# Optimization experiments

Hardware: AMD Instinct MI355X
Metric: run time of the kernel (lower is better)

The kernel has to match this reference:

```python
import jax, jax.numpy as jnp
import numpy as np


def setup_inputs() -> dict:
    key = jax.random.key(0)
    k1, k2, k3 = jax.random.split(key, 3)
    N1, N2, D = 2048, 32768, 1024
    return {
        "query_seq": jax.random.normal(k1, (N1, D), dtype=jnp.float32),
        "matching_set": jax.random.normal(k2, (N2, D), dtype=jnp.float32),
        "synth_set": jax.random.normal(k3, (N2, D), dtype=jnp.float32),
        "topk": 4,
    }


def reference(query_seq, matching_set, synth_set, topk):
    # fast_cosine_dist: the torch code computes dot products via the
    # -cdist^2 + ||a||^2 + ||b||^2 identity; mathematically this is q @ m^T.
    q_norm = jnp.linalg.norm(query_seq, axis=-1)        # [N1]
    m_norm = jnp.linalg.norm(matching_set, axis=-1)     # [N2]
    dotprod = jnp.einsum('nd,md->nm', query_seq, matching_set)  # [N1, N2]
    dists = 1.0 - dotprod / (q_norm[:, None] * m_norm[None, :])
    # topk smallest distances -> top_k of negated dists
    _, idx = jax.lax.top_k(-dists, topk)                # [N1, topk]
    out_feats = synth_set[idx].mean(axis=1)             # [N1, D]
    return out_feats
```

## Files before the change

### kernel.cpp

```cpp
#include <hip/hip_runtime.h>

#define N1 2048
#define N2 32768
#define DD 1024
#define BM 128
#define BN 128
#define BK 128
#define NBN (N2 / BN)
#define NBM (N1 / BM)
#define KT  (DD / BK)

typedef __attribute__((ext_vector_type(8))) int   i32x8;
typedef __attribute__((ext_vector_type(4))) int   i32x4;
typedef __attribute__((ext_vector_type(4))) float f32x4;

typedef const __attribute__((address_space(1))) void gv_t;
typedef __attribute__((address_space(3))) void       lv_t;

__device__ __forceinline__ void gload16(const void* g, void* l) {
  __builtin_amdgcn_global_load_lds((gv_t*)g, (lv_t*)l, 16, 0, 0);
}

__device__ __forceinline__ unsigned ordf(float x) {
  union { float f; unsigned u; } a; a.f = x;
  return a.u ^ ((unsigned)((int)a.u >> 31) | 0x80000000u);
}

__global__ __launch_bounds__(256) void nrmcvt8(const float* __restrict__ src,
                                               unsigned char* __restrict__ dst,
                                               float* __restrict__ invn) {
  const int row = blockIdx.x, t = threadIdx.x;
  const float4* s4 = (const float4*)(src + (size_t)row * DD);
  float4 v = s4[t];
  float ss = v.x * v.x + v.y * v.y + v.z * v.z + v.w * v.w;
  #pragma unroll
  for (int o = 32; o > 0; o >>= 1) ss += __shfl_down(ss, o, 64);
  __shared__ float red[4];
  if ((t & 63) == 0) red[t >> 6] = ss;
  __syncthreads();
  float inv = 1.0f / sqrtf(red[0] + red[1] + red[2] + red[3]);
  float sc = inv * 16.0f;
  int p = 0;
  p = __builtin_amdgcn_cvt_pk_fp8_f32(v.x * sc, v.y * sc, p, false);
  p = __builtin_amdgcn_cvt_pk_fp8_f32(v.z * sc, v.w * sc, p, true);
  ((unsigned*)(dst + (size_t)row * DD))[t] = (unsigned)p;
  if (invn != nullptr && t == 0) invn[row] = inv;
}

__global__ __launch_bounds__(256, 2) void gemm_topk(
    const unsigned char* __restrict__ qb,
    const unsigned char* __restrict__ mbn,
    unsigned* __restrict__ cand_k) {
  __shared__ char lds[65536];
  const int tid  = threadIdx.x;
  const int lane = tid & 63;
  const int w = tid >> 6, wr = w >> 1, wc = w & 1;

  int bid = blockIdx.x;
  int swz = (bid & 7) * (NBM * NBN / 8) + (bid >> 3);
  const int bm = swz >> 8;
  const int bn = swz & (NBN - 1);

  {
    int amt = (bid * 37) & 15;
    for (int k = 0; k < amt; ++k) __builtin_amdgcn_s_sleep(1);
  }

  const char* aG = (const char*)(qb  + (size_t)bm * BM * DD);
  const char* bG = (const char*)(mbn + (size_t)bn * BN * DD);

  f32x4 acc[4][4] = {};

  auto stage = [&](int d, int kt) {
    #pragma unroll
    for (int it = 0; it < 4; ++it) {
      int p = it * 256 + tid;
      int r = p >> 3, c = p & 7, cs = c ^ (r & 7);
      gload16(aG + (size_t)r * DD + kt * BK + cs * 16,
              lds + d * 32768 + p * 16);
    }
    #pragma unroll
    for (int it = 0; it < 4; ++it) {
      int p = it * 256 + tid;
      int r = p >> 3, c = p & 7, cs = c ^ (r & 7);
      gload16(bG + (size_t)r * DD + kt * BK + cs * 16,
              lds + d * 32768 + 16384 + p * 16);
    }
  };

  auto compute = [&](int d) {
    const char* Abuf = lds + d * 32768;
    const char* Bbuf = Abuf + 16384;
    const int g2 = 2 * (lane >> 4);
    i32x8 af[4], bb[4];
    #pragma unroll
    for (int i = 0; i < 4; ++i) {
      int ra = wr * 64 + i * 16 + (lane & 15);
      i32x4 lo = *(const i32x4*)(Abuf + ra * 128 + ((g2 ^ (ra & 7)) * 16));
      i32x4 hi = *(const i32x4*)(Abuf + ra * 128 + (((g2 + 1) ^ (ra & 7)) * 16));
      af[i] = __builtin_shufflevector(lo, hi, 0, 1, 2, 3, 4, 5, 6, 7);
      int rb = wc * 64 + i * 16 + (lane & 15);
      i32x4 blo = *(const i32x4*)(Bbuf + rb * 128 + ((g2 ^ (rb & 7)) * 16));
      i32x4 bhi = *(const i32x4*)(Bbuf + rb * 128 + (((g2 + 1) ^ (rb & 7)) * 16));
      bb[i] = __builtin_shufflevector(blo, bhi, 0, 1, 2, 3, 4, 5, 6, 7);
    }
    #pragma unroll
    for (int i = 0; i < 4; ++i)
      #pragma unroll
      for (int j = 0; j < 4; ++j)
        acc[i][j] = __builtin_amdgcn_mfma_scale_f32_16x16x128_f8f6f4(
            af[i], bb[j], acc[i][j], 0 , 0 ,
            0, 0x7F7F7F7F, 0, 0x7F7F7F7F );
  };

  stage(0, 0);
  __syncthreads();
  #pragma unroll 1
  for (int t = 0; t < KT; ++t) {
    if (t + 1 < KT) stage((t + 1) & 1, t + 1);
    compute(t & 1);
    __syncthreads();
  }

  float* sc = (float*)lds;
  #pragma unroll
  for (int i = 0; i < 4; ++i)
    #pragma unroll
    for (int j = 0; j < 4; ++j)
      #pragma unroll
      for (int q = 0; q < 4; ++q) {
        int r = wr * 64 + i * 16 + (lane >> 4) * 4 + q;
        int c = wc * 64 + j * 16 + (lane & 15);
        sc[r * 128 + ((c + r) & 127)] = acc[i][j][q];
      }
  __syncthreads();

  const int srow = tid >> 1, strip = tid & 1;
  unsigned k0 = 0, k1 = 0, k2 = 0, k3 = 0;
  for (int i = 0; i < 64; ++i) {
    int c = strip * 64 + i;
    float s = sc[srow * 128 + ((c + srow) & 127)];
    unsigned key = (ordf(s) & 0xFFFF8000u) | (unsigned)(bn * BN + c);
    unsigned b = key, t2;
    t2 = k0 < b ? k0 : b; k0 = k0 < b ? b : k0; b = t2;
    t2 = k1 < b ? k1 : b; k1 = k1 < b ? b : k1; b = t2;
    t2 = k2 < b ? k2 : b; k2 = k2 < b ? b : k2; b = t2;
    k3 = k3 < b ? b : k3;
  }
  unsigned* dst = cand_k + (size_t)(bm * BM + srow) * (NBN * 8) + bn * 8 + strip * 4;
  *(uint4*)dst = make_uint4(k0, k1, k2, k3);
}

__global__ __launch_bounds__(256) void finalize(
    const float* __restrict__ q, const float* __restrict__ m,
    const float* __restrict__ synth, const unsigned* __restrict__ cand_k,
    const float* __restrict__ inv_mn, float* __restrict__ out) {
  const int lane = threadIdx.x & 63;
  const int row  = blockIdx.x * 4 + (threadIdx.x >> 6);

  uint4 kk[8];
  const uint4* kp = (const uint4*)(cand_k + (size_t)row * (NBN * 8));
  #pragma unroll
  for (int ii = 0; ii < 8; ++ii) kk[ii] = kp[ii * 64 + lane];

  const float4* qp = (const float4*)(q + (size_t)row * DD);
  float4 qv[4];
  #pragma unroll
  for (int ph = 0; ph < 4; ++ph) qv[ph] = qp[ph * 64 + lane];

  unsigned wk[16];
  #pragma unroll
  for (int it = 0; it < 16; ++it) {
    unsigned lm = 0;
    #pragma unroll
    for (int ii = 0; ii < 8; ++ii) {
      unsigned a = kk[ii].x > kk[ii].y ? kk[ii].x : kk[ii].y;
      unsigned b = kk[ii].z > kk[ii].w ? kk[ii].z : kk[ii].w;
      a = a > b ? a : b;
      lm = lm > a ? lm : a;
    }
    #pragma unroll
    for (int o = 1; o < 64; o <<= 1) {
      unsigned other = (unsigned)__shfl_xor((int)lm, o, 64);
      lm = lm > other ? lm : other;
    }
    wk[it] = lm;
    #pragma unroll
    for (int ii = 0; ii < 8; ++ii) {
      kk[ii].x = kk[ii].x == lm ? 0u : kk[ii].x;
      kk[ii].y = kk[ii].y == lm ? 0u : kk[ii].y;
      kk[ii].z = kk[ii].z == lm ? 0u : kk[ii].z;
      kk[ii].w = kk[ii].w == lm ? 0u : kk[ii].w;
    }
  }

  float cosv[16]; int gidx[16];
  #pragma unroll
  for (int it = 0; it < 16; ++it) {
    int g = (int)(wk[it] & 0x7FFFu);
    gidx[it] = g;
    const float4* mp = (const float4*)(m + (size_t)g * DD);
    float d = 0.f;
    #pragma unroll
    for (int ph = 0; ph < 4; ++ph) {
      float4 mv = mp[ph * 64 + lane];
      d += mv.x * qv[ph].x + mv.y * qv[ph].y + mv.z * qv[ph].z + mv.w * qv[ph].w;
    }
    #pragma unroll
    for (int o = 1; o < 64; o <<= 1) d += __shfl_xor(d, o, 64);
    cosv[it] = d * inv_mn[g];
  }

  int sel[4]; bool used[16] = {};
  #pragma unroll
  for (int s = 0; s < 4; ++s) {
    float bv = -1e30f; int bg = 0x7FFFFFFF; int bj = -1;
    #pragma unroll
    for (int j = 0; j < 16; ++j) {
      bool better = !used[j] && (cosv[j] > bv || (cosv[j] == bv && gidx[j] < bg));
      bv = better ? cosv[j] : bv;
      bg = better ? gidx[j] : bg;
      bj = better ? j : bj;
    }
    sel[s] = bg;
    #pragma unroll
    for (int j = 0; j < 16; ++j) used[j] = used[j] || (j == bj);
  }

  const float4* s0 = (const float4*)(synth + (size_t)sel[0] * DD);
  const float4* s1 = (const float4*)(synth + (size_t)sel[1] * DD);
  const float4* s2 = (const float4*)(synth + (size_t)sel[2] * DD);
  const float4* s3 = (const float4*)(synth + (size_t)sel[3] * DD);
  float4* op = (float4*)(out + (size_t)row * DD);
  #pragma unroll
  for (int ph = 0; ph < 4; ++ph) {
    int ix = ph * 64 + lane;
    float4 a = s0[ix], b = s1[ix], c = s2[ix], d = s3[ix];
    float4 r;
    r.x = (a.x + b.x + c.x + d.x) * 0.25f;
    r.y = (a.y + b.y + c.y + d.y) * 0.25f;
    r.z = (a.z + b.z + c.z + d.z) * 0.25f;
    r.w = (a.w + b.w + c.w + d.w) * 0.25f;
    op[ix] = r;
  }
}

extern "C" void kernel_launch(void* const* d_in, const int* in_sizes, int n_in,
                              void* d_out, int out_size, void* d_ws, size_t ws_size,
                              hipStream_t stream) {
  (void)in_sizes; (void)n_in; (void)out_size; (void)ws_size;
  const float* q = (const float*)d_in[0];
  const float* m = (const float*)d_in[1];
  const float* s = (const float*)d_in[2];
  float* out = (float*)d_out;

  char* w = (char*)d_ws;
  unsigned char* qb     = (unsigned char*)w;
  unsigned char* mb     = (unsigned char*)(w + (2ull << 20));
  float*         inv_mn = (float*)(w + (40ull << 20));
  unsigned*      cand_k = (unsigned*)(w + (41ull << 20));

  nrmcvt8<<<N1, 256, 0, stream>>>(q, qb, nullptr);
  nrmcvt8<<<N2, 256, 0, stream>>>(m, mb, inv_mn);
  gemm_topk<<<NBM * NBN, 256, 0, stream>>>(qb, mb, cand_k);
  finalize<<<N1 / 4, 256, 0, stream>>>(q, m, s, cand_k, inv_mn, out);
}
```

Measured before the change: 181.3 us.

## Enlarge GEMM tile to 256x256 with 8 waves and split-barrier pipelining

Doubles the block tile to 256x256 with 512 threads (2x4 waves, each computing 128x64), halving global re-reads of the FP8 operands per output. The k-loop now issues the next stage's loads, waits with explicit vmcnt and raw barriers, and fences scheduling around compute. It also drops the staggered-start sleep and does the top-k epilogue in two halves through a 128 KB LDS buffer with XOR swizzle and vectorized reads. The cost is higher register pressure (32 accumulators) and full LDS use, so occupancy may fall and the grid drops to 1024 blocks.

```diff
diff --git a/kernel.cpp b/kernel.cpp
--- a/kernel.cpp
+++ b/kernel.cpp
@@ -3,12 +3,13 @@
 #define N1 2048
 #define N2 32768
 #define DD 1024
-#define BM 128
-#define BN 128
+#define BM 256
+#define BN 256
 #define BK 128
+#define NBM (N1 / BM)
 #define NBN (N2 / BN)
-#define NBM (N1 / BM)
 #define KT  (DD / BK)
+#define NKEY 2048
 
 typedef __attribute__((ext_vector_type(8))) int   i32x8;
 typedef __attribute__((ext_vector_type(4))) int   i32x4;
@@ -47,108 +48,125 @@
   if (invn != nullptr && t == 0) invn[row] = inv;
 }
 
-__global__ __launch_bounds__(256, 2) void gemm_topk(
+__global__ __launch_bounds__(512, 2) void gemm_topk(
     const unsigned char* __restrict__ qb,
     const unsigned char* __restrict__ mbn,
     unsigned* __restrict__ cand_k) {
-  __shared__ char lds[65536];
+  __shared__ char lds[131072];
   const int tid  = threadIdx.x;
   const int lane = tid & 63;
-  const int w = tid >> 6, wr = w >> 1, wc = w & 1;
+  const int w = tid >> 6, wr = w >> 2, wc = w & 3;
 
   int bid = blockIdx.x;
   int swz = (bid & 7) * (NBM * NBN / 8) + (bid >> 3);
-  const int bm = swz >> 8;
+  const int bm = swz >> 7;
   const int bn = swz & (NBN - 1);
-
-  {
-    int amt = (bid * 37) & 15;
-    for (int k = 0; k < amt; ++k) __builtin_amdgcn_s_sleep(1);
-  }
 
   const char* aG = (const char*)(qb  + (size_t)bm * BM * DD);
   const char* bG = (const char*)(mbn + (size_t)bn * BN * DD);
 
-  f32x4 acc[4][4] = {};
+  f32x4 acc[8][4] = {};
 
   auto stage = [&](int d, int kt) {
     #pragma unroll
     for (int it = 0; it < 4; ++it) {
-      int p = it * 256 + tid;
+      int p = it * 512 + tid;
       int r = p >> 3, c = p & 7, cs = c ^ (r & 7);
       gload16(aG + (size_t)r * DD + kt * BK + cs * 16,
-              lds + d * 32768 + p * 16);
+              lds + d * 65536 + p * 16);
     }
     #pragma unroll
     for (int it = 0; it < 4; ++it) {
-      int p = it * 256 + tid;
+      int p = it * 512 + tid;
       int r = p >> 3, c = p & 7, cs = c ^ (r & 7);
       gload16(bG + (size_t)r * DD + kt * BK + cs * 16,
-              lds + d * 32768 + 16384 + p * 16);
+              lds + d * 65536 + 32768 + p * 16);
     }
   };
 
   auto compute = [&](int d) {
-    const char* Abuf = lds + d * 32768;
-    const char* Bbuf = Abuf + 16384;
+    const char* Abuf = lds + d * 65536;
+    const char* Bbuf = Abuf + 32768;
     const int g2 = 2 * (lane >> 4);
-    i32x8 af[4], bb[4];
-    #pragma unroll
-    for (int i = 0; i < 4; ++i) {
-      int ra = wr * 64 + i * 16 + (lane & 15);
+    i32x8 bb[4];
+    #pragma unroll
+    for (int j = 0; j < 4; ++j) {
+      int rb = wc * 64 + j * 16 + (lane & 15);
+      i32x4 blo = *(const i32x4*)(Bbuf + rb * 128 + ((g2 ^ (rb & 7)) * 16));
+      i32x4 bhi = *(const i32x4*)(Bbuf + rb * 128 + (((g2 + 1) ^ (rb & 7)) * 16));
+      bb[j] = __builtin_shufflevector(blo, bhi, 0, 1, 2, 3, 4, 5, 6, 7);
+    }
+    #pragma unroll
+    for (int i = 0; i < 8; ++i) {
+      int ra = wr * 128 + i * 16 + (lane & 15);
       i32x4 lo = *(const i32x4*)(Abuf + ra * 128 + ((g2 ^ (ra & 7)) * 16));
       i32x4 hi = *(const i32x4*)(Abuf + ra * 128 + (((g2 + 1) ^ (ra & 7)) * 16));
-      af[i] = __builtin_shufflevector(lo, hi, 0, 1, 2, 3, 4, 5, 6, 7);
-      int rb = wc * 64 + i * 16 + (lane & 15);
-      i32x4 blo = *(const i32x4*)(Bbuf + rb * 128 + ((g2 ^ (rb & 7)) * 16));
-      i32x4 bhi = *(const i32x4*)(Bbuf + rb * 128 + (((g2 + 1) ^ (rb & 7)) * 16));
-      bb[i] = __builtin_shufflevector(blo, bhi, 0, 1, 2, 3, 4, 5, 6, 7);
-    }
-    #pragma unroll
-    for (int i = 0; i < 4; ++i)
+      i32x8 af = __builtin_shufflevector(lo, hi, 0, 1, 2, 3, 4, 5, 6, 7);
       #pragma unroll
       for (int j = 0; j < 4; ++j)
         acc[i][j] = __builtin_amdgcn_mfma_scale_f32_16x16x128_f8f6f4(
-            af[i], bb[j], acc[i][j], 0 , 0 ,
+            af, bb[j], acc[i][j], 0 , 0 ,
             0, 0x7F7F7F7F, 0, 0x7F7F7F7F );
+    }
   };
 
   stage(0, 0);
+  #pragma unroll 1
+  for (int t = 0; t < KT - 1; ++t) {
+    __builtin_amdgcn_s_barrier();
+    stage((t + 1) & 1, t + 1);
+    asm volatile("s_waitcnt vmcnt(8)" ::: "memory");
+    __builtin_amdgcn_s_barrier();
+    __builtin_amdgcn_sched_barrier(0);
+    compute(t & 1);
+  }
+  asm volatile("s_waitcnt vmcnt(0)" ::: "memory");
+  __builtin_amdgcn_s_barrier();
+  __builtin_amdgcn_sched_barrier(0);
+  compute((KT - 1) & 1);
   __syncthreads();
-  #pragma unroll 1
-  for (int t = 0; t < KT; ++t) {
-    if (t + 1 < KT) stage((t + 1) & 1, t + 1);
-    compute(t & 1);
+
+  for (int half = 0; half < 2; ++half) {
+    if (wr == half) {
+      float* sc = (float*)lds;
+      #pragma unroll
+      for (int i = 0; i < 8; ++i)
+        #pragma unroll
+        for (int q = 0; q < 4; ++q) {
+          int lr = i * 16 + (lane >> 4) * 4 + q;
+          #pragma unroll
+          for (int j = 0; j < 4; ++j) {
+            int c = wc * 64 + j * 16 + (lane & 15);
+            sc[lr * 256 + (c ^ ((lr & 15) << 2))] = acc[i][j][q];
+          }
+        }
+    }
     __syncthreads();
-  }
-
-  float* sc = (float*)lds;
-  #pragma unroll
-  for (int i = 0; i < 4; ++i)
-    #pragma unroll
-    for (int j = 0; j < 4; ++j)
+    {
+      const float* sc = (const float*)lds;
+      const int lr = tid >> 2, st = tid & 3;
+      unsigned k0 = 0, k1 = 0, k2 = 0, k3 = 0;
       #pragma unroll
-      for (int q = 0; q < 4; ++q) {
-        int r = wr * 64 + i * 16 + (lane >> 4) * 4 + q;
-        int c = wc * 64 + j * 16 + (lane & 15);
-        sc[r * 128 + ((c + r) & 127)] = acc[i][j][q];
+      for (int k4 = 0; k4 < 16; ++k4) {
+        int c0 = st * 64 + k4 * 4;
+        f32x4 v = *(const f32x4*)(sc + lr * 256 + (c0 ^ ((lr & 15) << 2)));
+        #pragma unroll
+        for (int e = 0; e < 4; ++e) {
+          unsigned key = (ordf(v[e]) & 0xFFFF8000u) |
+                         (unsigned)(bn * BN + c0 + e);
+          unsigned b = key, t2;
+          t2 = k0 < b ? k0 : b; k0 = k0 < b ? b : k0; b = t2;
+          t2 = k1 < b ? k1 : b; k1 = k1 < b ? b : k1; b = t2;
+          t2 = k2 < b ? k2 : b; k2 = k2 < b ? b : k2; b = t2;
+          k3 = k3 < b ? b : k3;
+        }
       }
-  __syncthreads();
-
-  const int srow = tid >> 1, strip = tid & 1;
-  unsigned k0 = 0, k1 = 0, k2 = 0, k3 = 0;
-  for (int i = 0; i < 64; ++i) {
-    int c = strip * 64 + i;
-    float s = sc[srow * 128 + ((c + srow) & 127)];
-    unsigned key = (ordf(s) & 0xFFFF8000u) | (unsigned)(bn * BN + c);
-    unsigned b = key, t2;
-    t2 = k0 < b ? k0 : b; k0 = k0 < b ? b : k0; b = t2;
-    t2 = k1 < b ? k1 : b; k1 = k1 < b ? b : k1; b = t2;
-    t2 = k2 < b ? k2 : b; k2 = k2 < b ? b : k2; b = t2;
-    k3 = k3 < b ? b : k3;
-  }
-  unsigned* dst = cand_k + (size_t)(bm * BM + srow) * (NBN * 8) + bn * 8 + strip * 4;
-  *(uint4*)dst = make_uint4(k0, k1, k2, k3);
+      int qrow = bm * BM + half * 128 + lr;
+      unsigned* dst = cand_k + (size_t)qrow * NKEY + (bn * 4 + st) * 4;
+      *(uint4*)dst = make_uint4(k0, k1, k2, k3);
+    }
+    __syncthreads();
+  }
 }
 
 __global__ __launch_bounds__(256) void finalize(
@@ -159,7 +177,7 @@
   const int row  = blockIdx.x * 4 + (threadIdx.x >> 6);
 
   uint4 kk[8];
-  const uint4* kp = (const uint4*)(cand_k + (size_t)row * (NBN * 8));
+  const uint4* kp = (const uint4*)(cand_k + (size_t)row * NKEY);
   #pragma unroll
   for (int ii = 0; ii < 8; ++ii) kk[ii] = kp[ii * 64 + lane];
 
@@ -262,6 +280,6 @@
 
   nrmcvt8<<<N1, 256, 0, stream>>>(q, qb, nullptr);
   nrmcvt8<<<N2, 256, 0, stream>>>(m, mb, inv_mn);
-  gemm_topk<<<NBM * NBN, 256, 0, stream>>>(qb, mb, cand_k);
+  gemm_topk<<<NBM * NBN, 512, 0, stream>>>(qb, mb, cand_k);
   finalize<<<N1 / 4, 256, 0, stream>>>(q, m, s, cand_k, inv_mn, out);
 }
```

Result: slower. 244.4 us (+34.8%).

## Pre-swizzle FP8 operands into MFMA layout and do per-wave register top-k

Applied to the files above, without the earlier changes.

The normalize/convert kernel now stages 16 rows in LDS and writes FP8 data pre-permuted into the MFMA fragment order. The GEMM keeps a 64-row query tile resident in LDS and streams matching-set fragments straight from global memory into registers, with no LDS double buffering. It keeps a running top-3 per row per lane in registers across 512 columns per wave, then merges these through LDS into a top-6 per strip. This removes the score write-back to LDS, the per-tile barriers and most candidate traffic, so finalize scans 384 candidates per row instead of 2048. In exchange, B operands are read directly from global with no reuse across waves, and the per-lane top-3 keeps fewer candidates, which could miss true neighbours when they cluster in one lane.

```diff
diff --git a/kernel.cpp b/kernel.cpp
--- a/kernel.cpp
+++ b/kernel.cpp
@@ -3,12 +3,7 @@
 #define N1 2048
 #define N2 32768
 #define DD 1024
-#define BM 128
-#define BN 128
-#define BK 128
-#define NBN (N2 / BN)
-#define NBM (N1 / BM)
-#define KT  (DD / BK)
+#define RS 1028
 
 typedef __attribute__((ext_vector_type(8))) int   i32x8;
 typedef __attribute__((ext_vector_type(4))) int   i32x4;
@@ -26,142 +21,178 @@
   return a.u ^ ((unsigned)((int)a.u >> 31) | 0x80000000u);
 }
 
-__global__ __launch_bounds__(256) void nrmcvt8(const float* __restrict__ src,
-                                               unsigned char* __restrict__ dst,
+__global__ __launch_bounds__(256) void nrmcvtT(const float* __restrict__ src,
+                                               unsigned char* __restrict__ dstT,
                                                float* __restrict__ invn) {
-  const int row = blockIdx.x, t = threadIdx.x;
-  const float4* s4 = (const float4*)(src + (size_t)row * DD);
-  float4 v = s4[t];
-  float ss = v.x * v.x + v.y * v.y + v.z * v.z + v.w * v.w;
-  #pragma unroll
-  for (int o = 32; o > 0; o >>= 1) ss += __shfl_down(ss, o, 64);
-  __shared__ float red[4];
-  if ((t & 63) == 0) red[t >> 6] = ss;
-  __syncthreads();
-  float inv = 1.0f / sqrtf(red[0] + red[1] + red[2] + red[3]);
-  float sc = inv * 16.0f;
-  int p = 0;
-  p = __builtin_amdgcn_cvt_pk_fp8_f32(v.x * sc, v.y * sc, p, false);
-  p = __builtin_amdgcn_cvt_pk_fp8_f32(v.z * sc, v.w * sc, p, true);
-  ((unsigned*)(dst + (size_t)row * DD))[t] = (unsigned)p;
-  if (invn != nullptr && t == 0) invn[row] = inv;
+  __shared__ float ldsf[16 * RS];
+  __shared__ float invs[16];
+  const int t = threadIdx.x, g = blockIdx.x;
+  const float4* s4 = (const float4*)(src + (size_t)g * 16 * DD);
+  #pragma unroll
+  for (int it = 0; it < 16; ++it) {
+    int p = it * 256 + t;
+    int row = p >> 8, c4 = p & 255;
+    *(float4*)(ldsf + row * RS + c4 * 4) = s4[p];
+  }
+  __syncthreads();
+  const int l = t & 63, w = t >> 6;
+  #pragma unroll
+  for (int rr = 0; rr < 4; ++rr) {
+    int row = w * 4 + rr;
+    float ss = 0.f;
+    #pragma unroll
+    for (int it = 0; it < 4; ++it) {
+      float4 v = *(const float4*)(ldsf + row * RS + (it * 64 + l) * 4);
+      ss += v.x * v.x + v.y * v.y + v.z * v.z + v.w * v.w;
+    }
+    #pragma unroll
+    for (int o = 32; o > 0; o >>= 1) ss += __shfl_down(ss, o, 64);
+    if (l == 0) {
+      float inv = 1.0f / sqrtf(ss);
+      invs[row] = inv;
+      if (invn != nullptr) invn[g * 16 + row] = inv;
+    }
+  }
+  __syncthreads();
+  unsigned* dst4 = (unsigned*)(dstT + (size_t)g * 16384);
+  #pragma unroll
+  for (int it = 0; it < 4; ++it) {
+    int p = it * 256 + t;
+    int L = p * 16;
+    int kt = L >> 11, hi = (L >> 10) & 1, idx = (L >> 4) & 63;
+    int qq = idx >> 4, r = idx & 15;
+    int k0 = kt * 128 + qq * 32 + hi * 16;
+    float sc = invs[r] * 16.0f;
+    uint4 o;
+    unsigned* op = (unsigned*)&o;
+    #pragma unroll
+    for (int e = 0; e < 4; ++e) {
+      float4 v = *(const float4*)(ldsf + r * RS + k0 + e * 4);
+      int pk = 0;
+      pk = __builtin_amdgcn_cvt_pk_fp8_f32(v.x * sc, v.y * sc, pk, false);
+      pk = __builtin_amdgcn_cvt_pk_fp8_f32(v.z * sc, v.w * sc, pk, true);
+      op[e] = (unsigned)pk;
+    }
+    *(uint4*)(dst4 + p * 4) = o;
+  }
 }
 
 __global__ __launch_bounds__(256, 2) void gemm_topk(
-    const unsigned char* __restrict__ qb,
-    const unsigned char* __restrict__ mbn,
-    unsigned* __restrict__ cand_k) {
+    const unsigned char* __restrict__ qbT,
+    const unsigned char* __restrict__ mbT,
+    unsigned* __restrict__ cand) {
   __shared__ char lds[65536];
-  const int tid  = threadIdx.x;
-  const int lane = tid & 63;
-  const int w = tid >> 6, wr = w >> 1, wc = w & 1;
-
-  int bid = blockIdx.x;
-  int swz = (bid & 7) * (NBM * NBN / 8) + (bid >> 3);
-  const int bm = swz >> 8;
-  const int bn = swz & (NBN - 1);
+  const int tid = threadIdx.x, l = tid & 63, w = tid >> 6;
+  const int qg = blockIdx.x >> 4;
+  const int nb = blockIdx.x & 15;
+  const int n0w = nb * 2048 + w * 512;
 
   {
-    int amt = (bid * 37) & 15;
-    for (int k = 0; k < amt; ++k) __builtin_amdgcn_s_sleep(1);
-  }
-
-  const char* aG = (const char*)(qb  + (size_t)bm * BM * DD);
-  const char* bG = (const char*)(mbn + (size_t)bn * BN * DD);
-
-  f32x4 acc[4][4] = {};
-
-  auto stage = [&](int d, int kt) {
-    #pragma unroll
-    for (int it = 0; it < 4; ++it) {
-      int p = it * 256 + tid;
-      int r = p >> 3, c = p & 7, cs = c ^ (r & 7);
-      gload16(aG + (size_t)r * DD + kt * BK + cs * 16,
-              lds + d * 32768 + p * 16);
-    }
-    #pragma unroll
-    for (int it = 0; it < 4; ++it) {
-      int p = it * 256 + tid;
-      int r = p >> 3, c = p & 7, cs = c ^ (r & 7);
-      gload16(bG + (size_t)r * DD + kt * BK + cs * 16,
-              lds + d * 32768 + 16384 + p * 16);
-    }
-  };
-
-  auto compute = [&](int d) {
-    const char* Abuf = lds + d * 32768;
-    const char* Bbuf = Abuf + 16384;
-    const int g2 = 2 * (lane >> 4);
-    i32x8 af[4], bb[4];
-    #pragma unroll
-    for (int i = 0; i < 4; ++i) {
-      int ra = wr * 64 + i * 16 + (lane & 15);
-      i32x4 lo = *(const i32x4*)(Abuf + ra * 128 + ((g2 ^ (ra & 7)) * 16));
-      i32x4 hi = *(const i32x4*)(Abuf + ra * 128 + (((g2 + 1) ^ (ra & 7)) * 16));
-      af[i] = __builtin_shufflevector(lo, hi, 0, 1, 2, 3, 4, 5, 6, 7);
-      int rb = wc * 64 + i * 16 + (lane & 15);
-      i32x4 blo = *(const i32x4*)(Bbuf + rb * 128 + ((g2 ^ (rb & 7)) * 16));
-      i32x4 bhi = *(const i32x4*)(Bbuf + rb * 128 + (((g2 + 1) ^ (rb & 7)) * 16));
-      bb[i] = __builtin_shufflevector(blo, bhi, 0, 1, 2, 3, 4, 5, 6, 7);
+    const char* src = (const char*)(qbT + (size_t)qg * 65536);
+    #pragma unroll
+    for (int it = 0; it < 16; ++it) {
+      int off = (it * 256 + tid) * 16;
+      gload16(src + off, lds + off);
+    }
+  }
+  __syncthreads();
+
+  unsigned keys[16][3];
+  #pragma unroll
+  for (int s = 0; s < 16; ++s) {
+    keys[s][0] = 0; keys[s][1] = 0; keys[s][2] = 0;
+  }
+
+  #pragma unroll 1
+  for (int nc = 0; nc < 8; ++nc) {
+    f32x4 acc[4][4] = {};
+    const char* mB = (const char*)mbT +
+                     (size_t)((n0w >> 4) + nc * 4) * 16384;
+    #pragma unroll
+    for (int kt = 0; kt < 8; ++kt) {
+      i32x8 bf[4], af[4];
+      #pragma unroll
+      for (int j = 0; j < 4; ++j) {
+        i32x4 lo = *(const i32x4*)(mB + j * 16384 + kt * 2048 + l * 16);
+        i32x4 hi = *(const i32x4*)(mB + j * 16384 + kt * 2048 + 1024 + l * 16);
+        bf[j] = __builtin_shufflevector(lo, hi, 0, 1, 2, 3, 4, 5, 6, 7);
+      }
+      #pragma unroll
+      for (int i = 0; i < 4; ++i) {
+        i32x4 lo = *(const i32x4*)(lds + (i * 8 + kt) * 2048 + l * 16);
+        i32x4 hi = *(const i32x4*)(lds + (i * 8 + kt) * 2048 + 1024 + l * 16);
+        af[i] = __builtin_shufflevector(lo, hi, 0, 1, 2, 3, 4, 5, 6, 7);
+      }
+      #pragma unroll
+      for (int i = 0; i < 4; ++i)
+        #pragma unroll
+        for (int j = 0; j < 4; ++j)
+          acc[i][j] = __builtin_amdgcn_mfma_scale_f32_16x16x128_f8f6f4(
+              af[i], bf[j], acc[i][j], 0 , 0 ,
+              0, 0x7F7F7F7F, 0, 0x7F7F7F7F );
     }
     #pragma unroll
     for (int i = 0; i < 4; ++i)
       #pragma unroll
       for (int j = 0; j < 4; ++j)
-        acc[i][j] = __builtin_amdgcn_mfma_scale_f32_16x16x128_f8f6f4(
-            af[i], bb[j], acc[i][j], 0 , 0 ,
-            0, 0x7F7F7F7F, 0, 0x7F7F7F7F );
-  };
-
-  stage(0, 0);
-  __syncthreads();
-  #pragma unroll 1
-  for (int t = 0; t < KT; ++t) {
-    if (t + 1 < KT) stage((t + 1) & 1, t + 1);
-    compute(t & 1);
-    __syncthreads();
-  }
-
-  float* sc = (float*)lds;
-  #pragma unroll
-  for (int i = 0; i < 4; ++i)
-    #pragma unroll
-    for (int j = 0; j < 4; ++j)
-      #pragma unroll
-      for (int q = 0; q < 4; ++q) {
-        int r = wr * 64 + i * 16 + (lane >> 4) * 4 + q;
-        int c = wc * 64 + j * 16 + (lane & 15);
-        sc[r * 128 + ((c + r) & 127)] = acc[i][j][q];
-      }
-  __syncthreads();
-
-  const int srow = tid >> 1, strip = tid & 1;
-  unsigned k0 = 0, k1 = 0, k2 = 0, k3 = 0;
-  for (int i = 0; i < 64; ++i) {
-    int c = strip * 64 + i;
-    float s = sc[srow * 128 + ((c + srow) & 127)];
-    unsigned key = (ordf(s) & 0xFFFF8000u) | (unsigned)(bn * BN + c);
-    unsigned b = key, t2;
-    t2 = k0 < b ? k0 : b; k0 = k0 < b ? b : k0; b = t2;
-    t2 = k1 < b ? k1 : b; k1 = k1 < b ? b : k1; b = t2;
-    t2 = k2 < b ? k2 : b; k2 = k2 < b ? b : k2; b = t2;
-    k3 = k3 < b ? b : k3;
-  }
-  unsigned* dst = cand_k + (size_t)(bm * BM + srow) * (NBN * 8) + bn * 8 + strip * 4;
-  *(uint4*)dst = make_uint4(k0, k1, k2, k3);
+        #pragma unroll
+        for (int r = 0; r < 4; ++r) {
+          unsigned key = (ordf(acc[i][j][r]) & 0xFFFF8000u) |
+                         (unsigned)(n0w + nc * 64 + j * 16 + (l & 15));
+          const int s = i * 4 + r;
+          unsigned b = key, t2;
+          t2 = keys[s][0] < b ? keys[s][0] : b;
+          keys[s][0] = keys[s][0] < b ? b : keys[s][0]; b = t2;
+          t2 = keys[s][1] < b ? keys[s][1] : b;
+          keys[s][1] = keys[s][1] < b ? b : keys[s][1]; b = t2;
+          keys[s][2] = keys[s][2] < b ? b : keys[s][2];
+        }
+  }
+
+  __syncthreads();
+  unsigned* ldsu = (unsigned*)lds;
+  #pragma unroll
+  for (int s = 0; s < 16; ++s) {
+    int r64 = (s >> 2) * 16 + (l >> 4) * 4 + (s & 3);
+    int base = (w * 64 + r64) * 49 + (l & 15) * 3;
+    ldsu[base + 0] = keys[s][0];
+    ldsu[base + 1] = keys[s][1];
+    ldsu[base + 2] = keys[s][2];
+  }
+  __syncthreads();
+  {
+    int w2 = tid >> 6, r = tid & 63;
+    const unsigned* kp = ldsu + (w2 * 64 + r) * 49;
+    unsigned m0 = 0, m1 = 0, m2 = 0, m3 = 0, m4 = 0, m5 = 0;
+    #pragma unroll
+    for (int k = 0; k < 48; ++k) {
+      unsigned b = kp[k], t2;
+      t2 = m0 < b ? m0 : b; m0 = m0 < b ? b : m0; b = t2;
+      t2 = m1 < b ? m1 : b; m1 = m1 < b ? b : m1; b = t2;
+      t2 = m2 < b ? m2 : b; m2 = m2 < b ? b : m2; b = t2;
+      t2 = m3 < b ? m3 : b; m3 = m3 < b ? b : m3; b = t2;
+      t2 = m4 < b ? m4 : b; m4 = m4 < b ? b : m4; b = t2;
+      m5 = m5 < b ? b : m5;
+    }
+    int row = qg * 64 + r;
+    int strip = nb * 4 + w2;
+    unsigned* dst = cand + (size_t)row * 384 + strip * 6;
+    dst[0] = m0; dst[1] = m1; dst[2] = m2;
+    dst[3] = m3; dst[4] = m4; dst[5] = m5;
+  }
 }
 
 __global__ __launch_bounds__(256) void finalize(
     const float* __restrict__ q, const float* __restrict__ m,
-    const float* __restrict__ synth, const unsigned* __restrict__ cand_k,
+    const float* __restrict__ synth, const unsigned* __restrict__ cand,
     const float* __restrict__ inv_mn, float* __restrict__ out) {
   const int lane = threadIdx.x & 63;
   const int row  = blockIdx.x * 4 + (threadIdx.x >> 6);
 
-  uint4 kk[8];
-  const uint4* kp = (const uint4*)(cand_k + (size_t)row * (NBN * 8));
-  #pragma unroll
-  for (int ii = 0; ii < 8; ++ii) kk[ii] = kp[ii * 64 + lane];
+  unsigned kk[6];
+  const unsigned* kp = cand + (size_t)row * 384 + lane * 6;
+  #pragma unroll
+  for (int d = 0; d < 6; ++d) kk[d] = kp[d];
 
   const float4* qp = (const float4*)(q + (size_t)row * DD);
   float4 qv[4];
@@ -173,12 +204,7 @@
   for (int it = 0; it < 16; ++it) {
     unsigned lm = 0;
     #pragma unroll
-    for (int ii = 0; ii < 8; ++ii) {
-      unsigned a = kk[ii].x > kk[ii].y ? kk[ii].x : kk[ii].y;
-      unsigned b = kk[ii].z > kk[ii].w ? kk[ii].z : kk[ii].w;
-      a = a > b ? a : b;
-      lm = lm > a ? lm : a;
-    }
+    for (int d = 0; d < 6; ++d) lm = lm > kk[d] ? lm : kk[d];
     #pragma unroll
     for (int o = 1; o < 64; o <<= 1) {
       unsigned other = (unsigned)__shfl_xor((int)lm, o, 64);
@@ -186,12 +212,7 @@
     }
     wk[it] = lm;
     #pragma unroll
-    for (int ii = 0; ii < 8; ++ii) {
-      kk[ii].x = kk[ii].x == lm ? 0u : kk[ii].x;
-      kk[ii].y = kk[ii].y == lm ? 0u : kk[ii].y;
-      kk[ii].z = kk[ii].z == lm ? 0u : kk[ii].z;
-      kk[ii].w = kk[ii].w == lm ? 0u : kk[ii].w;
-    }
+    for (int d = 0; d < 6; ++d) kk[d] = (kk[d] == lm) ? 0u : kk[d];
   }
 
   float cosv[16]; int gidx[16];
@@ -254,14 +275,14 @@
   const float* s = (const float*)d_in[2];
   float* out = (float*)d_out;
 
-  char* w = (char*)d_ws;
-  unsigned char* qb     = (unsigned char*)w;
-  unsigned char* mb     = (unsigned char*)(w + (2ull << 20));
-  float*         inv_mn = (float*)(w + (40ull << 20));
-  unsigned*      cand_k = (unsigned*)(w + (41ull << 20));
-
-  nrmcvt8<<<N1, 256, 0, stream>>>(q, qb, nullptr);
-  nrmcvt8<<<N2, 256, 0, stream>>>(m, mb, inv_mn);
-  gemm_topk<<<NBM * NBN, 256, 0, stream>>>(qb, mb, cand_k);
-  finalize<<<N1 / 4, 256, 0, stream>>>(q, m, s, cand_k, inv_mn, out);
-}
+  char* wsp = (char*)d_ws;
+  unsigned char* qbT    = (unsigned char*)wsp;
+  unsigned char* mbT    = (unsigned char*)(wsp + (4ull << 20));
+  float*         inv_mn = (float*)(wsp + (40ull << 20));
+  unsigned*      cand   = (unsigned*)(wsp + (41ull << 20));
+
+  nrmcvtT<<<N1 / 16, 256, 0, stream>>>(q, qbT, nullptr);
+  nrmcvtT<<<N2 / 16, 256, 0, stream>>>(m, mbT, inv_mn);
+  gemm_topk<<<(N1 / 64) * (N2 / 2048), 256, 0, stream>>>(qbT, mbT, cand);
+  finalize<<<N1 / 4, 256, 0, stream>>>(q, m, s, cand, inv_mn, out);
+}
```

After: 242.2 us. 33.6% more time.
